# Performance work log

Hardware: AMD Instinct MI355X
Metric: run time of the kernel (lower is better)

Reference implementation:

```python
import jax, jax.numpy as jnp
import numpy as np

N = 50000      # nodes
E = 800000     # edges
D = 64         # input_dim = hidden_dim = output_dim
ED = 16        # edge_attr dim
L = 4          # total GATConv layers (2 per GAT block)
G = 64         # number of graphs in the batch vector
NEG_SLOPE = 0.2


def setup_inputs() -> dict:
    key = jax.random.key(0)
    ks = jax.random.split(key, 12)
    s = 0.1
    x = jax.random.normal(ks[0], (N, D), jnp.float32)
    edge_index = jax.random.randint(ks[1], (2, E), 0, N, jnp.int32)
    edge_attr = jax.random.normal(ks[2], (E, ED), jnp.float32)
    batch = jnp.sort(jax.random.randint(ks[3], (N,), 0, G, jnp.int32))
    return {
        "x": x,
        "edge_index": edge_index,
        "edge_attr": edge_attr,
        "batch": batch,
        # stacked per-layer GATConv params (all layers are D->D)
        "W": jax.random.normal(ks[4], (L, D, D), jnp.float32) * s,
        "a_src": jax.random.normal(ks[5], (L, D), jnp.float32) * s,
        "a_dst": jax.random.normal(ks[6], (L, D), jnp.float32) * s,
        "We": jax.random.normal(ks[7], (L, ED, D), jnp.float32) * s,
        "a_e": jax.random.normal(ks[8], (L, D), jnp.float32) * s,
        "b": jnp.zeros((L, D), jnp.float32),
        "Wfc": jax.random.normal(ks[9], (D, 2048), jnp.float32) * s,
        "bfc": jnp.zeros((2048,), jnp.float32),
    }


def _gat_conv(h, src, dst, edge_attr, W, a_s, a_d, We, a_e, b):
    # single-head GATConv with edge features (PyG semantics, flow src->dst)
    hw = h @ W                                      # [N, D]
    el = (edge_attr @ We) @ a_e                     # [E]
    score = jax.nn.leaky_relu(
        (hw @ a_s)[src] + (hw @ a_d)[dst] + el, NEG_SLOPE)  # [E]
    # softmax over incoming edges of each dst node
    m = jax.ops.segment_max(score, dst, num_segments=N)      # [N]
    p = jnp.exp(score - m[dst])                               # [E]
    denom = jax.ops.segment_sum(p, dst, num_segments=N)      # [N]
    alpha = p / denom[dst]                                    # [E]
    out = jax.ops.segment_sum(alpha[:, None] * hw[src], dst, num_segments=N)
    return out + b


def reference(x, edge_index, edge_attr, batch, W, a_src, a_dst, We, a_e, b, Wfc, bfc):
    src, dst = edge_index[0], edge_index[1]
    h = x
    for l in range(L):
        h = _gat_conv(h, src, dst, edge_attr,
                      W[l], a_src[l], a_dst[l], We[l], a_e[l], b[l])
        if l < L - 1:  # relu inside blocks and between the two GAT blocks
            h = jax.nn.relu(h)
    # global_mean_pool over batch vector
    counts = jax.ops.segment_sum(jnp.ones((N,), h.dtype), batch, num_segments=G)
    pooled = jax.ops.segment_sum(h, batch, num_segments=G) / jnp.maximum(counts, 1.0)[:, None]
    out = pooled @ Wfc + bfc                        # [G, 2048]
    return out[None]                                # stacked over list -> [1, G, 2048]
```

## Files before the change

kernel.cpp:

```cpp
#include <hip/hip_runtime.h>
#include <hip/hip_bf16.h>

#define NN 50000
#define EE 800000
#define DD 64
#define LL 4
#define GG 64
#define PJ 16

__global__ __launch_bounds__(256) void k_el(const float* __restrict__ ea,
                                            const float* __restrict__ We,
                                            const float* __restrict__ a_e,
                                            const int* __restrict__ dst,
                                            int* __restrict__ counts,
                                            float* __restrict__ el_all, int ne) {
    __shared__ float sce[64];
    if (threadIdx.x < 64) {
        int l = threadIdx.x >> 4, k = threadIdx.x & 15;
        float acc = 0.f;
        for (int j = 0; j < 64; ++j)
            acc += We[l * 1024 + k * 64 + j] * a_e[l * 64 + j];
        sce[threadIdx.x] = acc;
    }
    __syncthreads();
    int e = blockIdx.x * 256 + threadIdx.x;
    if (e >= ne) return;
    atomicAdd(&counts[dst[e]], 1);
    const float4* p4 = reinterpret_cast<const float4*>(ea + (size_t)e * 16);
    float v[16];
    float4 q;
    q = p4[0]; v[0] = q.x; v[1] = q.y; v[2] = q.z; v[3] = q.w;
    q = p4[1]; v[4] = q.x; v[5] = q.y; v[6] = q.z; v[7] = q.w;
    q = p4[2]; v[8] = q.x; v[9] = q.y; v[10] = q.z; v[11] = q.w;
    q = p4[3]; v[12] = q.x; v[13] = q.y; v[14] = q.z; v[15] = q.w;
    float o[4];
#pragma unroll
    for (int l = 0; l < 4; ++l) {
        float a = 0.f;
#pragma unroll
        for (int k = 0; k < 16; ++k) a = fmaf(v[k], sce[l * 16 + k], a);
        o[l] = a;
    }
    reinterpret_cast<float4*>(el_all)[e] = make_float4(o[0], o[1], o[2], o[3]);
}

__global__ void k_scan1(const int* __restrict__ counts, int* __restrict__ bsum, int n) {
    __shared__ int s[256];
    int i = blockIdx.x * 256 + threadIdx.x;
    s[threadIdx.x] = (i < n) ? counts[i] : 0;
    __syncthreads();
    for (int off = 128; off; off >>= 1) {
        if (threadIdx.x < off) s[threadIdx.x] += s[threadIdx.x + off];
        __syncthreads();
    }
    if (threadIdx.x == 0) bsum[blockIdx.x] = s[0];
}

__global__ void k_scan2(int* __restrict__ bsum, int nb) {
    __shared__ int s[256];
    int t = threadIdx.x;
    int v = (t < nb) ? bsum[t] : 0;
    s[t] = v;
    __syncthreads();
    for (int off = 1; off < 256; off <<= 1) {
        int x = (t >= off) ? s[t - off] : 0;
        __syncthreads();
        s[t] += x;
        __syncthreads();
    }
    if (t < nb) bsum[t] = s[t] - v;
}

__global__ void k_scan3(const int* __restrict__ counts, const int* __restrict__ bsum,
                        int* __restrict__ row_ptr, int n) {
    __shared__ int s[256];
    int t = threadIdx.x;
    int i = blockIdx.x * 256 + t;
    int v = (i < n) ? counts[i] : 0;
    s[t] = v;
    __syncthreads();
    for (int off = 1; off < 256; off <<= 1) {
        int x = (t >= off) ? s[t - off] : 0;
        __syncthreads();
        s[t] += x;
        __syncthreads();
    }
    if (i < n) row_ptr[i] = s[t] - v + bsum[blockIdx.x];
}

__global__ void k_fill(const int* __restrict__ dst,
                       const int* __restrict__ row_ptr, int* __restrict__ cursor,
                       int* __restrict__ csr_eid, int ne) {
    int e = blockIdx.x * 256 + threadIdx.x;
    if (e >= ne) return;
    int d = dst[e];
    int pos = row_ptr[d] + atomicAdd(&cursor[d], 1);
    csr_eid[pos] = e;
}

__global__ __launch_bounds__(256) void k_sortperm(int* __restrict__ csr_eid,
                                                  const int* __restrict__ e_src,
                                                  const int* __restrict__ row_ptr,
                                                  const int* __restrict__ counts,
                                                  const float4* __restrict__ el_all,
                                                  int2* __restrict__ p0, int2* __restrict__ p1,
                                                  int2* __restrict__ p2, int2* __restrict__ p3,
                                                  int n) {
    int wid = threadIdx.x >> 6, lane = threadIdx.x & 63;
    int nd = blockIdx.x * 4 + wid;
    if (nd >= n) return;
    int s = row_ptr[nd], d = counts[nd];
    if (d == 0) return;
    if (d <= 64) {
        int eid = 0x7FFFFFFF;
        if (lane < d) eid = csr_eid[s + lane];
        int rank = 0;
        for (int j = 0; j < d; ++j) {
            int ej = __shfl(eid, j, 64);
            rank += (ej < eid) ? 1 : 0;
        }
        if (lane < d) {
            int sr = e_src[eid];
            float4 ev = el_all[eid];
            p0[s + rank] = make_int2(sr, __float_as_int(ev.x));
            p1[s + rank] = make_int2(sr, __float_as_int(ev.y));
            p2[s + rank] = make_int2(sr, __float_as_int(ev.z));
            p3[s + rank] = make_int2(sr, __float_as_int(ev.w));
        }
    } else if (lane == 0) {
        for (int i = 1; i < d; ++i) {
            int key = csr_eid[s + i];
            int j = i - 1;
            while (j >= 0 && csr_eid[s + j] > key) {
                csr_eid[s + j + 1] = csr_eid[s + j];
                --j;
            }
            csr_eid[s + j + 1] = key;
        }
        for (int i = 0; i < d; ++i) {
            int eid = csr_eid[s + i];
            int sr = e_src[eid];
            float4 ev = el_all[eid];
            p0[s + i] = make_int2(sr, __float_as_int(ev.x));
            p1[s + i] = make_int2(sr, __float_as_int(ev.y));
            p2[s + i] = make_int2(sr, __float_as_int(ev.z));
            p3[s + i] = make_int2(sr, __float_as_int(ev.w));
        }
    }
}

__global__ __launch_bounds__(256) void k_gemm(const float* __restrict__ h,
                                              const float* __restrict__ W,
                                              const float* __restrict__ a_s,
                                              const float* __restrict__ a_d,
                                              float* __restrict__ hw,
                                              float* __restrict__ ssrc,
                                              float* __restrict__ sdst, int n) {
    __shared__ float sHT[64 * 68];
    __shared__ float sW[64 * 64];
    int t = threadIdx.x;
    int nbase = blockIdx.x * 64;
    int nrem = n - nbase;
    const float4* W4 = (const float4*)W;
    float4* sW4 = (float4*)sW;
#pragma unroll
    for (int p = 0; p < 4; ++p) sW4[t + p * 256] = W4[t + p * 256];
#pragma unroll
    for (int p = 0; p < 4; ++p) {
        int idx = t + p * 256;
        int node = idx >> 4, d4 = idx & 15;
        float4 v = make_float4(0.f, 0.f, 0.f, 0.f);
        if (node < nrem) v = ((const float4*)(h + (size_t)(nbase + node) * 64))[d4];
        sHT[(d4 * 4 + 0) * 68 + node] = v.x;
        sHT[(d4 * 4 + 1) * 68 + node] = v.y;
        sHT[(d4 * 4 + 2) * 68 + node] = v.z;
        sHT[(d4 * 4 + 3) * 68 + node] = v.w;
    }
    __syncthreads();
    int nr = (t >> 4) * 4;
    int nc = (t & 15) * 4;
    float a0[4], a1[4], a2[4], a3[4];
#pragma unroll
    for (int j = 0; j < 4; ++j) { a0[j] = 0.f; a1[j] = 0.f; a2[j] = 0.f; a3[j] = 0.f; }
    for (int k = 0; k < 64; ++k) {
        float4 hv = *(const float4*)&sHT[k * 68 + nr];
        float4 wv = *(const float4*)&sW[k * 64 + nc];
        a0[0] = fmaf(hv.x, wv.x, a0[0]); a0[1] = fmaf(hv.x, wv.y, a0[1]);
        a0[2] = fmaf(hv.x, wv.z, a0[2]); a0[3] = fmaf(hv.x, wv.w, a0[3]);
        a1[0] = fmaf(hv.y, wv.x, a1[0]); a1[1] = fmaf(hv.y, wv.y, a1[1]);
        a1[2] = fmaf(hv.y, wv.z, a1[2]); a1[3] = fmaf(hv.y, wv.w, a1[3]);
        a2[0] = fmaf(hv.z, wv.x, a2[0]); a2[1] = fmaf(hv.z, wv.y, a2[1]);
        a2[2] = fmaf(hv.z, wv.z, a2[2]); a2[3] = fmaf(hv.z, wv.w, a2[3]);
        a3[0] = fmaf(hv.w, wv.x, a3[0]); a3[1] = fmaf(hv.w, wv.y, a3[1]);
        a3[2] = fmaf(hv.w, wv.z, a3[2]); a3[3] = fmaf(hv.w, wv.w, a3[3]);
    }
    if (nr + 0 < nrem) ((float4*)(hw + (size_t)(nbase + nr + 0) * 64))[t & 15] =
        make_float4(a0[0], a0[1], a0[2], a0[3]);
    if (nr + 1 < nrem) ((float4*)(hw + (size_t)(nbase + nr + 1) * 64))[t & 15] =
        make_float4(a1[0], a1[1], a1[2], a1[3]);
    if (nr + 2 < nrem) ((float4*)(hw + (size_t)(nbase + nr + 2) * 64))[t & 15] =
        make_float4(a2[0], a2[1], a2[2], a2[3]);
    if (nr + 3 < nrem) ((float4*)(hw + (size_t)(nbase + nr + 3) * 64))[t & 15] =
        make_float4(a3[0], a3[1], a3[2], a3[3]);
    float as0 = a_s[nc], as1 = a_s[nc + 1], as2 = a_s[nc + 2], as3 = a_s[nc + 3];
    float ad0 = a_d[nc], ad1 = a_d[nc + 1], ad2 = a_d[nc + 2], ad3 = a_d[nc + 3];
    float ts0 = fmaf(a0[3], as3, fmaf(a0[2], as2, fmaf(a0[1], as1, a0[0] * as0)));
    float ts1 = fmaf(a1[3], as3, fmaf(a1[2], as2, fmaf(a1[1], as1, a1[0] * as0)));
    float ts2 = fmaf(a2[3], as3, fmaf(a2[2], as2, fmaf(a2[1], as1, a2[0] * as0)));
    float ts3 = fmaf(a3[3], as3, fmaf(a3[2], as2, fmaf(a3[1], as1, a3[0] * as0)));
    float td0 = fmaf(a0[3], ad3, fmaf(a0[2], ad2, fmaf(a0[1], ad1, a0[0] * ad0)));
    float td1 = fmaf(a1[3], ad3, fmaf(a1[2], ad2, fmaf(a1[1], ad1, a1[0] * ad0)));
    float td2 = fmaf(a2[3], ad3, fmaf(a2[2], ad2, fmaf(a2[1], ad1, a2[0] * ad0)));
    float td3 = fmaf(a3[3], ad3, fmaf(a3[2], ad2, fmaf(a3[1], ad1, a3[0] * ad0)));
#pragma unroll
    for (int off = 1; off < 16; off <<= 1) {
        ts0 += __shfl_xor(ts0, off, 64); ts1 += __shfl_xor(ts1, off, 64);
        ts2 += __shfl_xor(ts2, off, 64); ts3 += __shfl_xor(ts3, off, 64);
        td0 += __shfl_xor(td0, off, 64); td1 += __shfl_xor(td1, off, 64);
        td2 += __shfl_xor(td2, off, 64); td3 += __shfl_xor(td3, off, 64);
    }
    if ((t & 15) == 0) {
        if (nr + 0 < nrem) { ssrc[nbase + nr + 0] = ts0; sdst[nbase + nr + 0] = td0; }
        if (nr + 1 < nrem) { ssrc[nbase + nr + 1] = ts1; sdst[nbase + nr + 1] = td1; }
        if (nr + 2 < nrem) { ssrc[nbase + nr + 2] = ts2; sdst[nbase + nr + 2] = td2; }
        if (nr + 3 < nrem) { ssrc[nbase + nr + 3] = ts3; sdst[nbase + nr + 3] = td3; }
    }
}

__global__ __launch_bounds__(256) void k_row(const float* __restrict__ hw,
                                             const float* __restrict__ ssrc,
                                             const float* __restrict__ sdstA,
                                             const int2* __restrict__ plane,
                                             const int* __restrict__ row_ptr,
                                             const int* __restrict__ counts,
                                             const float* __restrict__ bias,
                                             int relu_flag, float* __restrict__ hout, int n) {
    int wid = threadIdx.x >> 6, lane = threadIdx.x & 63;
    int nd = blockIdx.x * 4 + wid;
    if (nd >= n) return;
    int start = row_ptr[nd], deg = counts[nd];
    if (deg == 0) {
        float outv = bias[lane];
        if (relu_flag) outv = fmaxf(outv, 0.f);
        hout[(size_t)nd * 64 + lane] = outv;
        return;
    }
    if (deg <= 64) {
        float sdn = sdstA[nd];
        int p = start + lane;
        int s_l = 0;
        float sc = -INFINITY;
        if (lane < deg) {
            int2 se = plane[p];
            s_l = se.x;
            sc = ssrc[s_l] + sdn + __int_as_float(se.y);
            sc = sc > 0.f ? sc : 0.2f * sc;
        }
        float mx = sc;
#pragma unroll
        for (int off = 32; off; off >>= 1) mx = fmaxf(mx, __shfl_xor(mx, off, 64));
        float pe = (lane < deg) ? __expf(sc - mx) : 0.f;
        float dsum = pe;
#pragma unroll
        for (int off = 32; off; off >>= 1) dsum += __shfl_xor(dsum, off, 64);
        const float* hwL = hw + lane;
        float acc = 0.f;
        float v0 = 0.f, v1 = 0.f, v2 = 0.f, v3 = 0.f,
              v4 = 0.f, v5 = 0.f, v6 = 0.f, v7 = 0.f;
        {
            int t0 = __shfl(s_l, 0, 64), t1 = __shfl(s_l, 1, 64);
            int t2 = __shfl(s_l, 2, 64), t3 = __shfl(s_l, 3, 64);
            int t4 = __shfl(s_l, 4, 64), t5 = __shfl(s_l, 5, 64);
            int t6 = __shfl(s_l, 6, 64), t7 = __shfl(s_l, 7, 64);
            if (0 < deg) v0 = hwL[(size_t)t0 * 64];
            if (1 < deg) v1 = hwL[(size_t)t1 * 64];
            if (2 < deg) v2 = hwL[(size_t)t2 * 64];
            if (3 < deg) v3 = hwL[(size_t)t3 * 64];
            if (4 < deg) v4 = hwL[(size_t)t4 * 64];
            if (5 < deg) v5 = hwL[(size_t)t5 * 64];
            if (6 < deg) v6 = hwL[(size_t)t6 * 64];
            if (7 < deg) v7 = hwL[(size_t)t7 * 64];
        }
        for (int i = 0; i < deg; i += 8) {
            float p0 = __shfl(pe, i, 64),     p1 = __shfl(pe, (i + 1) & 63, 64);
            float p2 = __shfl(pe, (i + 2) & 63, 64), p3 = __shfl(pe, (i + 3) & 63, 64);
            float p4 = __shfl(pe, (i + 4) & 63, 64), p5 = __shfl(pe, (i + 5) & 63, 64);
            float p6 = __shfl(pe, (i + 6) & 63, 64), p7 = __shfl(pe, (i + 7) & 63, 64);
            int t0 = __shfl(s_l, (i + 8) & 63, 64),  t1 = __shfl(s_l, (i + 9) & 63, 64);
            int t2 = __shfl(s_l, (i + 10) & 63, 64), t3 = __shfl(s_l, (i + 11) & 63, 64);
            int t4 = __shfl(s_l, (i + 12) & 63, 64), t5 = __shfl(s_l, (i + 13) & 63, 64);
            int t6 = __shfl(s_l, (i + 14) & 63, 64), t7 = __shfl(s_l, (i + 15) & 63, 64);
            float w0 = v0, w1 = v1, w2 = v2, w3 = v3,
                  w4 = v4, w5 = v5, w6 = v6, w7 = v7;
            if (i + 8 < deg)  v0 = hwL[(size_t)t0 * 64];
            if (i + 9 < deg)  v1 = hwL[(size_t)t1 * 64];
            if (i + 10 < deg) v2 = hwL[(size_t)t2 * 64];
            if (i + 11 < deg) v3 = hwL[(size_t)t3 * 64];
            if (i + 12 < deg) v4 = hwL[(size_t)t4 * 64];
            if (i + 13 < deg) v5 = hwL[(size_t)t5 * 64];
            if (i + 14 < deg) v6 = hwL[(size_t)t6 * 64];
            if (i + 15 < deg) v7 = hwL[(size_t)t7 * 64];
            acc = fmaf(p0, w0, acc);
            if (i + 1 < deg) acc = fmaf(p1, w1, acc);
            if (i + 2 < deg) acc = fmaf(p2, w2, acc);
            if (i + 3 < deg) acc = fmaf(p3, w3, acc);
            if (i + 4 < deg) acc = fmaf(p4, w4, acc);
            if (i + 5 < deg) acc = fmaf(p5, w5, acc);
            if (i + 6 < deg) acc = fmaf(p6, w6, acc);
            if (i + 7 < deg) acc = fmaf(p7, w7, acc);
        }
        float outv = acc / dsum + bias[lane];
        if (relu_flag) outv = fmaxf(outv, 0.f);
        hout[(size_t)nd * 64 + lane] = outv;
        return;
    }
    {
        float sdn = sdstA[nd];
        float mx = -INFINITY;
        for (int i = lane; i < deg; i += 64) {
            int2 se = plane[start + i];
            float sc = ssrc[se.x] + sdn + __int_as_float(se.y);
            sc = sc > 0.f ? sc : 0.2f * sc;
            mx = fmaxf(mx, sc);
        }
#pragma unroll
        for (int off = 32; off; off >>= 1) mx = fmaxf(mx, __shfl_xor(mx, off, 64));
        float dsum = 0.f;
        for (int i = lane; i < deg; i += 64) {
            int2 se = plane[start + i];
            float sc = ssrc[se.x] + sdn + __int_as_float(se.y);
            sc = sc > 0.f ? sc : 0.2f * sc;
            dsum += __expf(sc - mx);
        }
#pragma unroll
        for (int off = 32; off; off >>= 1) dsum += __shfl_xor(dsum, off, 64);
        float acc = 0.f;
        for (int i = 0; i < deg; ++i) {
            int2 se = plane[start + i];
            float sc = ssrc[se.x] + sdn + __int_as_float(se.y);
            sc = sc > 0.f ? sc : 0.2f * sc;
            float pex = __expf(sc - mx);
            acc = fmaf(pex, hw[(size_t)se.x * 64 + lane], acc);
        }
        float outv = acc / dsum + bias[lane];
        if (relu_flag) outv = fmaxf(outv, 0.f);
        hout[(size_t)nd * 64 + lane] = outv;
    }
}

__global__ __launch_bounds__(256) void k_pool_part(const float* __restrict__ h,
                                                   const int* __restrict__ batch,
                                                   float* __restrict__ partial, int n) {
    int g = blockIdx.y, j = blockIdx.x;
    int lo = 0, hi = n;
    while (lo < hi) { int mid = (lo + hi) >> 1; if (batch[mid] < g) lo = mid + 1; else hi = mid; }
    int start = lo;
    lo = start; hi = n;
    while (lo < hi) { int mid = (lo + hi) >> 1; if (batch[mid] < g + 1) lo = mid + 1; else hi = mid; }
    int end = lo;
    int cnt = end - start;
    int chunk = (cnt + PJ - 1) / PJ;
    int clo = start + j * chunk;
    int chi = min(clo + chunk, end);
    int lane = threadIdx.x & 63, q = threadIdx.x >> 6;
    float acc = 0.f;
    for (int nd = clo + q; nd < chi; nd += 4) acc += h[(size_t)nd * 64 + lane];
    __shared__ float s[4][64];
    s[q][lane] = acc;
    __syncthreads();
    if (threadIdx.x < 64) {
        float tot = s[0][threadIdx.x] + s[1][threadIdx.x] + s[2][threadIdx.x] + s[3][threadIdx.x];
        partial[((size_t)g * PJ + j) * 64 + threadIdx.x] = tot;
    }
}

__global__ __launch_bounds__(256) void k_fc(const float* __restrict__ partial,
                                            const int* __restrict__ batch,
                                            const float* __restrict__ Wfc,
                                            const float* __restrict__ bfc,
                                            float* __restrict__ out, int n) {
    int g = blockIdx.y;
    int c = blockIdx.x * 256 + threadIdx.x;
    __shared__ float sp[64];
    if (threadIdx.x < 64) {
        int d = threadIdx.x;
        float tot = 0.f;
#pragma unroll
        for (int j = 0; j < PJ; ++j) tot += partial[((size_t)g * PJ + j) * 64 + d];
        int lo = 0, hi = n;
        while (lo < hi) { int mid = (lo + hi) >> 1; if (batch[mid] < g) lo = mid + 1; else hi = mid; }
        int start = lo;
        lo = start; hi = n;
        while (lo < hi) { int mid = (lo + hi) >> 1; if (batch[mid] < g + 1) lo = mid + 1; else hi = mid; }
        int cnt = lo - start;
        sp[d] = tot / fmaxf((float)cnt, 1.0f);
    }
    __syncthreads();
    float acc = bfc[c];
#pragma unroll
    for (int k = 0; k < 64; ++k) acc = fmaf(sp[k], Wfc[k * 2048 + c], acc);
    out[(size_t)g * 2048 + c] = acc;
}

extern "C" void kernel_launch(void* const* d_in, const int* in_sizes, int n_in,
                              void* d_out, int out_size, void* d_ws, size_t ws_size,
                              hipStream_t stream) {
    const float* x = (const float*)d_in[0];
    const int* edge_index = (const int*)d_in[1];
    const float* edge_attr = (const float*)d_in[2];
    const int* batch = (const int*)d_in[3];
    const float* W = (const float*)d_in[4];
    const float* a_src = (const float*)d_in[5];
    const float* a_dst = (const float*)d_in[6];
    const float* We = (const float*)d_in[7];
    const float* a_e = (const float*)d_in[8];
    const float* b = (const float*)d_in[9];
    const float* Wfc = (const float*)d_in[10];
    const float* bfc = (const float*)d_in[11];
    float* out = (float*)d_out;

    char* ws = (char*)d_ws;
    size_t off = 0;
    auto alloc = [&](size_t bytes) {
        void* p = ws + off;
        off = (off + bytes + 255) & ~(size_t)255;
        return p;
    };
    float* h0      = (float*)alloc((size_t)NN * 64 * 4);
    float* h1      = (float*)alloc((size_t)NN * 64 * 4);
    float* hw      = (float*)alloc((size_t)NN * 64 * 4);
    float* ssrc    = (float*)alloc((size_t)NN * 4);
    float* sdst    = (float*)alloc((size_t)NN * 4);
    float* el_all  = (float*)alloc((size_t)EE * 16);
    int2*  planes  = (int2*)alloc((size_t)EE * 8 * 4);
    int*   csr_eid = (int*)alloc((size_t)EE * 4);
    int*   counts  = (int*)alloc((size_t)NN * 4);
    int*   row_ptr = (int*)alloc((size_t)NN * 4);
    int*   cursor  = (int*)alloc((size_t)NN * 4);
    int*   bsum    = (int*)alloc(256 * 4);
    float* partial = (float*)alloc((size_t)GG * PJ * 64 * 4);
    (void)ws_size; (void)in_sizes; (void)n_in; (void)out_size;

    const int* e_src = edge_index;
    const int* e_dst = edge_index + EE;
    const int EB = EE / 256;
    const int NB = (NN + 255) / 256;

    hipMemsetAsync(counts, 0, (size_t)NN * 4, stream);
    hipMemsetAsync(cursor, 0, (size_t)NN * 4, stream);

    k_el<<<EB, 256, 0, stream>>>(edge_attr, We, a_e, e_dst, counts, el_all, EE);
    k_scan1<<<NB, 256, 0, stream>>>(counts, bsum, NN);
    k_scan2<<<1, 256, 0, stream>>>(bsum, NB);
    k_scan3<<<NB, 256, 0, stream>>>(counts, bsum, row_ptr, NN);
    k_fill<<<EB, 256, 0, stream>>>(e_dst, row_ptr, cursor, csr_eid, EE);
    k_sortperm<<<(NN + 3) / 4, 256, 0, stream>>>(csr_eid, e_src, row_ptr, counts,
                                                 (const float4*)el_all,
                                                 planes, planes + EE,
                                                 planes + 2 * (size_t)EE,
                                                 planes + 3 * (size_t)EE, NN);

    const float* hin = x;
    float* hbufs[2] = {h0, h1};
    for (int l = 0; l < LL; ++l) {
        k_gemm<<<(NN + 63) / 64, 256, 0, stream>>>(hin, W + l * 4096, a_src + l * 64,
                                                   a_dst + l * 64, hw, ssrc, sdst, NN);
        float* hout = hbufs[l & 1];
        k_row<<<(NN + 3) / 4, 256, 0, stream>>>(hw, ssrc, sdst, planes + (size_t)l * EE,
                                                row_ptr, counts,
                                                b + l * 64, (l < LL - 1) ? 1 : 0, hout, NN);
        hin = hout;
    }
    k_pool_part<<<dim3(PJ, GG), 256, 0, stream>>>(hin, batch, partial, NN);
    k_fc<<<dim3(2048 / 256, GG), 256, 0, stream>>>(partial, batch, Wfc, bfc, out, NN);
}
```

Baseline: 372.0 us.

## Split edge planes into shared src index and per-layer score arrays; partition fill by XCD

Replaces the four per-layer interleaved (src, edge-score) int2 planes with one shared CSR source-index array plus four separate float edge-score arrays. This cuts the bytes written in the sort/permute pass. The edge-fill kernel is also launched over an extra grid dimension of 8 destination ranges, so each block only performs atomics for destinations in its range, aiming to keep cursor atomics local to one XCD's cache. The cost is that every edge is read 8 times in the fill kernel, and k_row now makes two loads per edge instead of one.

```diff
diff --git a/kernel.cpp b/kernel.cpp
--- a/kernel.cpp
+++ b/kernel.cpp
@@ -7,6 +7,8 @@
 #define LL 4
 #define GG 64
 #define PJ 16
+#define NXCD 8
+#define DRANGE (NN / NXCD)
 
 __global__ __launch_bounds__(256) void k_el(const float* __restrict__ ea,
                                             const float* __restrict__ We,
@@ -88,12 +90,16 @@
     if (i < n) row_ptr[i] = s[t] - v + bsum[blockIdx.x];
 }
 
-__global__ void k_fill(const int* __restrict__ dst,
-                       const int* __restrict__ row_ptr, int* __restrict__ cursor,
-                       int* __restrict__ csr_eid, int ne) {
-    int e = blockIdx.x * 256 + threadIdx.x;
+__global__ __launch_bounds__(256) void k_fill(const int* __restrict__ dst,
+                                              const int* __restrict__ row_ptr,
+                                              int* __restrict__ cursor,
+                                              int* __restrict__ csr_eid, int ne) {
+    int r = blockIdx.x;
+    int e = blockIdx.y * 256 + threadIdx.x;
     if (e >= ne) return;
     int d = dst[e];
+    int rlo = r * DRANGE;
+    if (d < rlo || d >= rlo + DRANGE) return;
     int pos = row_ptr[d] + atomicAdd(&cursor[d], 1);
     csr_eid[pos] = e;
 }
@@ -103,8 +109,9 @@
                                                   const int* __restrict__ row_ptr,
                                                   const int* __restrict__ counts,
                                                   const float4* __restrict__ el_all,
-                                                  int2* __restrict__ p0, int2* __restrict__ p1,
-                                                  int2* __restrict__ p2, int2* __restrict__ p3,
+                                                  int* __restrict__ csr_src,
+                                                  float* __restrict__ e0, float* __restrict__ e1,
+                                                  float* __restrict__ e2, float* __restrict__ e3,
                                                   int n) {
     int wid = threadIdx.x >> 6, lane = threadIdx.x & 63;
     int nd = blockIdx.x * 4 + wid;
@@ -122,10 +129,9 @@
         if (lane < d) {
             int sr = e_src[eid];
             float4 ev = el_all[eid];
-            p0[s + rank] = make_int2(sr, __float_as_int(ev.x));
-            p1[s + rank] = make_int2(sr, __float_as_int(ev.y));
-            p2[s + rank] = make_int2(sr, __float_as_int(ev.z));
-            p3[s + rank] = make_int2(sr, __float_as_int(ev.w));
+            csr_src[s + rank] = sr;
+            e0[s + rank] = ev.x; e1[s + rank] = ev.y;
+            e2[s + rank] = ev.z; e3[s + rank] = ev.w;
         }
     } else if (lane == 0) {
         for (int i = 1; i < d; ++i) {
@@ -139,12 +145,9 @@
         }
         for (int i = 0; i < d; ++i) {
             int eid = csr_eid[s + i];
-            int sr = e_src[eid];
             float4 ev = el_all[eid];
-            p0[s + i] = make_int2(sr, __float_as_int(ev.x));
-            p1[s + i] = make_int2(sr, __float_as_int(ev.y));
-            p2[s + i] = make_int2(sr, __float_as_int(ev.z));
-            p3[s + i] = make_int2(sr, __float_as_int(ev.w));
+            csr_src[s + i] = e_src[eid];
+            e0[s + i] = ev.x; e1[s + i] = ev.y; e2[s + i] = ev.z; e3[s + i] = ev.w;
         }
     }
 }
@@ -230,7 +233,8 @@
 __global__ __launch_bounds__(256) void k_row(const float* __restrict__ hw,
                                              const float* __restrict__ ssrc,
                                              const float* __restrict__ sdstA,
-                                             const int2* __restrict__ plane,
+                                             const int* __restrict__ csr_src,
+                                             const float* __restrict__ elpL,
                                              const int* __restrict__ row_ptr,
                                              const int* __restrict__ counts,
                                              const float* __restrict__ bias,
@@ -251,9 +255,8 @@
         int s_l = 0;
         float sc = -INFINITY;
         if (lane < deg) {
-            int2 se = plane[p];
-            s_l = se.x;
-            sc = ssrc[s_l] + sdn + __int_as_float(se.y);
+            s_l = csr_src[p];
+            sc = ssrc[s_l] + sdn + elpL[p];
             sc = sc > 0.f ? sc : 0.2f * sc;
         }
         float mx = sc;
@@ -318,8 +321,8 @@
         float sdn = sdstA[nd];
         float mx = -INFINITY;
         for (int i = lane; i < deg; i += 64) {
-            int2 se = plane[start + i];
-            float sc = ssrc[se.x] + sdn + __int_as_float(se.y);
+            int p = start + i;
+            float sc = ssrc[csr_src[p]] + sdn + elpL[p];
             sc = sc > 0.f ? sc : 0.2f * sc;
             mx = fmaxf(mx, sc);
         }
@@ -327,8 +330,8 @@
         for (int off = 32; off; off >>= 1) mx = fmaxf(mx, __shfl_xor(mx, off, 64));
         float dsum = 0.f;
         for (int i = lane; i < deg; i += 64) {
-            int2 se = plane[start + i];
-            float sc = ssrc[se.x] + sdn + __int_as_float(se.y);
+            int p = start + i;
+            float sc = ssrc[csr_src[p]] + sdn + elpL[p];
             sc = sc > 0.f ? sc : 0.2f * sc;
             dsum += __expf(sc - mx);
         }
@@ -336,11 +339,12 @@
         for (int off = 32; off; off >>= 1) dsum += __shfl_xor(dsum, off, 64);
         float acc = 0.f;
         for (int i = 0; i < deg; ++i) {
-            int2 se = plane[start + i];
-            float sc = ssrc[se.x] + sdn + __int_as_float(se.y);
+            int p = start + i;
+            int s = csr_src[p];
+            float sc = ssrc[s] + sdn + elpL[p];
             sc = sc > 0.f ? sc : 0.2f * sc;
             float pex = __expf(sc - mx);
-            acc = fmaf(pex, hw[(size_t)se.x * 64 + lane], acc);
+            acc = fmaf(pex, hw[(size_t)s * 64 + lane], acc);
         }
         float outv = acc / dsum + bias[lane];
         if (relu_flag) outv = fmaxf(outv, 0.f);
@@ -432,7 +436,8 @@
     float* ssrc    = (float*)alloc((size_t)NN * 4);
     float* sdst    = (float*)alloc((size_t)NN * 4);
     float* el_all  = (float*)alloc((size_t)EE * 16);
-    int2*  planes  = (int2*)alloc((size_t)EE * 8 * 4);
+    float* elpT    = (float*)alloc((size_t)EE * 4 * 4);
+    int*   csr_src = (int*)alloc((size_t)EE * 4);
     int*   csr_eid = (int*)alloc((size_t)EE * 4);
     int*   counts  = (int*)alloc((size_t)NN * 4);
     int*   row_ptr = (int*)alloc((size_t)NN * 4);
@@ -453,12 +458,11 @@
     k_scan1<<<NB, 256, 0, stream>>>(counts, bsum, NN);
     k_scan2<<<1, 256, 0, stream>>>(bsum, NB);
     k_scan3<<<NB, 256, 0, stream>>>(counts, bsum, row_ptr, NN);
-    k_fill<<<EB, 256, 0, stream>>>(e_dst, row_ptr, cursor, csr_eid, EE);
+    k_fill<<<dim3(NXCD, EB), 256, 0, stream>>>(e_dst, row_ptr, cursor, csr_eid, EE);
     k_sortperm<<<(NN + 3) / 4, 256, 0, stream>>>(csr_eid, e_src, row_ptr, counts,
-                                                 (const float4*)el_all,
-                                                 planes, planes + EE,
-                                                 planes + 2 * (size_t)EE,
-                                                 planes + 3 * (size_t)EE, NN);
+                                                 (const float4*)el_all, csr_src,
+                                                 elpT, elpT + EE, elpT + 2 * (size_t)EE,
+                                                 elpT + 3 * (size_t)EE, NN);
 
     const float* hin = x;
     float* hbufs[2] = {h0, h1};
@@ -466,8 +470,8 @@
         k_gemm<<<(NN + 63) / 64, 256, 0, stream>>>(hin, W + l * 4096, a_src + l * 64,
                                                    a_dst + l * 64, hw, ssrc, sdst, NN);
         float* hout = hbufs[l & 1];
-        k_row<<<(NN + 3) / 4, 256, 0, stream>>>(hw, ssrc, sdst, planes + (size_t)l * EE,
-                                                row_ptr, counts,
+        k_row<<<(NN + 3) / 4, 256, 0, stream>>>(hw, ssrc, sdst, csr_src,
+                                                elpT + (size_t)l * EE, row_ptr, counts,
                                                 b + l * 64, (l < LL - 1) ? 1 : 0, hout, NN);
         hin = hout;
     }
```

New measurement: 366.5 us. About the same (-1.5%).
